# Kernel tuning notes

Measured on AMD Instinct MI355X. Metric: run time of the kernel, lower is better.

The kernel has to match this reference:

```python
import jax, jax.numpy as jnp
import numpy as np

B, N_FEAT, D = 16384, 32, 64
HID1, HID2, HOF = 1024, 512, 64
OUT = 1
N_PAIRS = N_FEAT * (N_FEAT - 1) // 2
EPS = 1e-5


def setup_inputs() -> dict:
    key = jax.random.key(0)
    ks = jax.random.split(key, 16)
    s = 0.02
    return {
        "x": jax.random.normal(ks[0], (B, N_FEAT, D), dtype=jnp.float32),
        "W1": jax.random.normal(ks[1], (N_FEAT * D, HID1), dtype=jnp.float32) * s,
        "b1": jnp.zeros((HID1,), jnp.float32),
        "g1": jnp.ones((HID1,), jnp.float32),
        "beta1": jnp.zeros((HID1,), jnp.float32),
        "W2": jax.random.normal(ks[2], (HID1, HID2), dtype=jnp.float32) * s,
        "b2": jnp.zeros((HID2,), jnp.float32),
        "g2": jnp.ones((HID2,), jnp.float32),
        "beta2": jnp.zeros((HID2,), jnp.float32),
        "W3": jax.random.normal(ks[3], (HID2, HOF), dtype=jnp.float32) * s,
        "b3": jnp.zeros((HOF,), jnp.float32),
        "Wc": jax.random.normal(ks[4], (HOF + N_PAIRS, OUT), dtype=jnp.float32) * s,
        "bc": jnp.zeros((OUT,), jnp.float32),
    }


def _batchnorm(h, g, beta):
    # BatchNorm1d in training mode: batch mean / biased variance
    m = jnp.mean(h, axis=0)
    v = jnp.var(h, axis=0)
    return g * (h - m) * jax.lax.rsqrt(v + EPS) + beta


_IU, _JU = np.triu_indices(N_FEAT, k=1)  # same (i<j) order as nested loop


def reference(x, W1, b1, g1, beta1, W2, b2, g2, beta2, W3, b3, Wc, bc):
    # second-order interactions: all pairwise dot products, gathered upper-tri
    gram = jnp.einsum("bnd,bmd->bnm", x, x)          # [B, N, N]
    pairs = gram[:, _IU, _JU]                          # [B, N*(N-1)/2]
    # deep processor
    flat = x.reshape(x.shape[0], -1)                   # [B, N*D]
    h = _batchnorm(jax.nn.relu(flat @ W1 + b1), g1, beta1)
    h = _batchnorm(jax.nn.relu(h @ W2 + b2), g2, beta2)
    hof = h @ W3 + b3                                  # [B, HOF]
    inter = jnp.concatenate([hof, pairs], axis=1)
    return inter @ Wc + bc
```

## Files before the change

kernel.cpp:

```cpp
#include <hip/hip_runtime.h>
#include <stdint.h>

typedef unsigned short u16;
typedef unsigned char u8;
typedef __attribute__((ext_vector_type(8))) short short8;
typedef __attribute__((ext_vector_type(4))) float f32x4;
typedef __attribute__((ext_vector_type(16))) float f32x16;
typedef __attribute__((ext_vector_type(4))) int i32x4;
typedef __attribute__((ext_vector_type(8))) int i32x8;

#define BATCH 16384L
#define WSCALE 64.0f
#define INV_WSCALE (1.0f / 64.0f)
#define SCALE_ONE 0x7f7f7f7f
#define INVB (1.0f / 16384.0f)

__device__ __forceinline__ u16 f2bf_trunc(float f) {
    union { float f; uint32_t u; } cv; cv.f = f;
    return (u16)(cv.u >> 16);
}
__device__ __forceinline__ float bf2f(u16 h) {
    union { uint32_t u; float f; } cv; cv.u = ((uint32_t)h) << 16;
    return cv.f;
}
template<bool HI>
__device__ __forceinline__ uint32_t fp8pk(float a, float b, uint32_t old) {
    return (uint32_t)__builtin_amdgcn_cvt_pk_fp8_f32(a, b, (int)old, HI);
}
__device__ __forceinline__ u8 f2fp8(float v) {
    return (u8)(__builtin_amdgcn_cvt_pk_fp8_f32(v, v, 0, false) & 0xff);
}

__global__ __launch_bounds__(256) void k_gram(const float* __restrict__ x,
                                              const float* __restrict__ Wc,
                                              const float* __restrict__ W1,
                                              u8* __restrict__ xb,
                                              u8* __restrict__ w1f,
                                              float* __restrict__ spair,
                                              float* __restrict__ stats) {
    if (blockIdx.x >= 4096) {
        __shared__ float tile[32][33];
        const int bid2 = blockIdx.x - 4096;
        const int nb = (bid2 & 31) * 32;
        const int kb = (bid2 >> 5) * 32;
        const int tx = threadIdx.x & 31, ty = threadIdx.x >> 5;
        for (int r = ty; r < 32; r += 8)
            tile[r][tx] = W1[(long)(kb + r) * 1024 + nb + tx];
        __syncthreads();
        for (int r = ty; r < 32; r += 8)
            w1f[(long)(nb + r) * 2048 + kb + tx] = f2fp8(WSCALE * tile[tx][r]);
        return;
    }
    if (blockIdx.x == 0) {
        for (int j = threadIdx.x; j < 3072; j += 256) stats[j] = 0.f;
    }
    const int wave = threadIdx.x >> 6;
    const int lane = threadIdx.x & 63;
    const long b = (long)blockIdx.x * 4 + wave;
    const int r16 = lane & 15, quad = lane >> 4;
    const float* xg = x + b * 2048;

    short8 hi[2][2], lo[2][2];
    for (int mt = 0; mt < 2; mt++) {
        for (int k0 = 0; k0 < 2; k0++) {
            const int row = mt * 16 + r16;
            const int kof = k0 * 32 + quad * 8;
            const float* p = xg + row * 64 + kof;
            float4 p0 = *(const float4*)p;
            float4 p1 = *(const float4*)(p + 4);
            float v[8] = {p0.x, p0.y, p0.z, p0.w, p1.x, p1.y, p1.z, p1.w};
            short8 h, l;
            for (int j = 0; j < 8; j++) {
                u16 hb = f2bf_trunc(v[j]);
                h[j] = (short)hb;
                l[j] = (short)f2bf_trunc(v[j] - bf2f(hb));
            }
            hi[mt][k0] = h; lo[mt][k0] = l;
            uint32_t w0 = fp8pk<false>(v[0], v[1], 0); w0 = fp8pk<true>(v[2], v[3], w0);
            uint32_t w1 = fp8pk<false>(v[4], v[5], 0); w1 = fp8pk<true>(v[6], v[7], w1);
            *(uint2*)(xb + b * 2048 + row * 64 + kof) = make_uint2(w0, w1);
        }
    }
    f32x4 zero = {0.f, 0.f, 0.f, 0.f};
    f32x4 acc[2][2];
    for (int mt = 0; mt < 2; mt++) for (int nt = 0; nt < 2; nt++) acc[mt][nt] = zero;
    for (int k0 = 0; k0 < 2; k0++)
        for (int mt = 0; mt < 2; mt++)
            for (int nt = 0; nt < 2; nt++) {
                acc[mt][nt] = __builtin_amdgcn_mfma_f32_16x16x32_bf16(hi[mt][k0], hi[nt][k0], acc[mt][nt], 0, 0, 0);
                acc[mt][nt] = __builtin_amdgcn_mfma_f32_16x16x32_bf16(hi[mt][k0], lo[nt][k0], acc[mt][nt], 0, 0, 0);
                acc[mt][nt] = __builtin_amdgcn_mfma_f32_16x16x32_bf16(lo[mt][k0], hi[nt][k0], acc[mt][nt], 0, 0, 0);
            }
    float pacc = 0.f;
    for (int mt = 0; mt < 2; mt++)
        for (int nt = 0; nt < 2; nt++)
            for (int r = 0; r < 4; r++) {
                int row = mt * 16 + quad * 4 + r;
                int col = nt * 16 + r16;
                if (col > row) {
                    int p = 31 * row - (row * (row - 1)) / 2 + (col - row - 1);
                    pacc += acc[mt][nt][r] * Wc[64 + p];
                }
            }
    for (int off = 1; off < 64; off <<= 1) pacc += __shfl_xor(pacc, off);
    if (lane == 0) spair[b] = pacc;
}

__device__ __forceinline__ i32x8 frag32(const u8* __restrict__ lds, int R, int cb) {
    const int s = R & 7;
    i32x4 lo = *(const i32x4*)&lds[R * 128 + ((cb ^ s) * 16)];
    i32x4 hi = *(const i32x4*)&lds[R * 128 + (((cb + 1) ^ s) * 16)];
    i32x8 r;
    r[0] = lo[0]; r[1] = lo[1]; r[2] = lo[2]; r[3] = lo[3];
    r[4] = hi[0]; r[5] = hi[1]; r[6] = hi[2]; r[7] = hi[3];
    return r;
}

template<int LOGNB>
__global__ __launch_bounds__(512) void gemm_bn8(const u8* __restrict__ A,
                                                const u8* __restrict__ Bt,
                                                const float* __restrict__ bias,
                                                u8* __restrict__ C,
                                                float* __restrict__ sums,
                                                float* __restrict__ ssq,
                                                int N, int K, float inv) {
    __shared__ u8 lA[2][32768];
    __shared__ u8 lB[2][32768];
    const int tid = threadIdx.x;
    const int lane = tid & 63, wave = tid >> 6;
    const int wm = wave >> 2, wn = wave & 3;
    const int r32 = lane & 31, hf = lane >> 5;
    const int lid = blockIdx.x;
    const int xcd = lid & 7, t = lid >> 3;
    const int nbk = t & ((1 << LOGNB) - 1);
    const int mbk = xcd * (32 >> LOGNB) + (t >> LOGNB);
    const long m0 = (long)mbk * 256;
    const long n0 = (long)nbk * 256;

    const u8* srcA[4]; const u8* srcB[4]; int dstc[4];
#pragma unroll
    for (int i = 0; i < 4; i++) {
        const int c = tid + 512 * i;
        const int row = c >> 3, pos = c & 7;
        const int g = pos ^ (row & 7);
        srcA[i] = A + (m0 + row) * (long)K + g * 16;
        srcB[i] = Bt + (n0 + row) * (long)K + g * 16;
        dstc[i] = c * 16;
    }

    f32x16 acc[4][2];
#pragma unroll
    for (int mt = 0; mt < 4; mt++)
#pragma unroll
        for (int nt = 0; nt < 2; nt++)
#pragma unroll
            for (int r = 0; r < 16; r++) acc[mt][nt][r] = 0.f;

#pragma unroll
    for (int i = 0; i < 4; i++)
        __builtin_amdgcn_global_load_lds((const __attribute__((address_space(1))) void*)srcA[i],
                                         (__attribute__((address_space(3))) void*)(&lA[0][dstc[i]]), 16, 0, 0);
#pragma unroll
    for (int i = 0; i < 4; i++)
        __builtin_amdgcn_global_load_lds((const __attribute__((address_space(1))) void*)srcB[i],
                                         (__attribute__((address_space(3))) void*)(&lB[0][dstc[i]]), 16, 0, 0);
    __syncthreads();

    const int NT = K >> 7;
    for (int ti = 0; ti < NT; ti++) {
        const int cur = ti & 1, nxt = cur ^ 1;
        const long koff = (long)(ti + 1) << 7;
        const bool pf = (ti + 1 < NT);
        const u8* la = &lA[cur][0];
        const u8* lb = &lB[cur][0];
        i32x8 af[4], bf;

#pragma unroll
        for (int mt = 0; mt < 4; mt++)
            af[mt] = frag32(la, wm * 128 + mt * 32 + r32, hf * 2);
        bf = frag32(lb, wn * 64 + r32, hf * 2);
        if (pf) {
#pragma unroll
            for (int i = 0; i < 4; i++)
                __builtin_amdgcn_global_load_lds((const __attribute__((address_space(1))) void*)(srcA[i] + koff),
                                                 (__attribute__((address_space(3))) void*)(&lA[nxt][dstc[i]]), 16, 0, 0);
        }
        __builtin_amdgcn_s_barrier();
        asm volatile("s_waitcnt lgkmcnt(0)" ::: "memory");
        __builtin_amdgcn_sched_barrier(0);
        __builtin_amdgcn_s_setprio(1);
#pragma unroll
        for (int mt = 0; mt < 4; mt++)
            acc[mt][0] = __builtin_amdgcn_mfma_scale_f32_32x32x64_f8f6f4(
                af[mt], bf, acc[mt][0], 0, 0, 0, SCALE_ONE, 0, SCALE_ONE);
        __builtin_amdgcn_s_setprio(0);
        __builtin_amdgcn_s_barrier();

        bf = frag32(lb, wn * 64 + 32 + r32, hf * 2);
        if (pf) {
#pragma unroll
            for (int i = 0; i < 4; i++)
                __builtin_amdgcn_global_load_lds((const __attribute__((address_space(1))) void*)(srcB[i] + koff),
                                                 (__attribute__((address_space(3))) void*)(&lB[nxt][dstc[i]]), 16, 0, 0);
        }
        __builtin_amdgcn_s_barrier();
        asm volatile("s_waitcnt lgkmcnt(0)" ::: "memory");
        __builtin_amdgcn_sched_barrier(0);
        __builtin_amdgcn_s_setprio(1);
#pragma unroll
        for (int mt = 0; mt < 4; mt++)
            acc[mt][1] = __builtin_amdgcn_mfma_scale_f32_32x32x64_f8f6f4(
                af[mt], bf, acc[mt][1], 0, 0, 0, SCALE_ONE, 0, SCALE_ONE);
        __builtin_amdgcn_s_setprio(0);
        __builtin_amdgcn_s_barrier();

#pragma unroll
        for (int mt = 0; mt < 4; mt++)
            af[mt] = frag32(la, wm * 128 + mt * 32 + r32, 4 + hf * 2);
        bf = frag32(lb, wn * 64 + r32, 4 + hf * 2);
        __builtin_amdgcn_s_barrier();
        asm volatile("s_waitcnt lgkmcnt(0)" ::: "memory");
        __builtin_amdgcn_sched_barrier(0);
        __builtin_amdgcn_s_setprio(1);
#pragma unroll
        for (int mt = 0; mt < 4; mt++)
            acc[mt][0] = __builtin_amdgcn_mfma_scale_f32_32x32x64_f8f6f4(
                af[mt], bf, acc[mt][0], 0, 0, 0, SCALE_ONE, 0, SCALE_ONE);
        __builtin_amdgcn_s_setprio(0);
        __builtin_amdgcn_s_barrier();

        bf = frag32(lb, wn * 64 + 32 + r32, 4 + hf * 2);
        __builtin_amdgcn_s_barrier();
        asm volatile("s_waitcnt lgkmcnt(0)" ::: "memory");
        __builtin_amdgcn_sched_barrier(0);
        __builtin_amdgcn_s_setprio(1);
#pragma unroll
        for (int mt = 0; mt < 4; mt++)
            acc[mt][1] = __builtin_amdgcn_mfma_scale_f32_32x32x64_f8f6f4(
                af[mt], bf, acc[mt][1], 0, 0, 0, SCALE_ONE, 0, SCALE_ONE);
        __builtin_amdgcn_s_setprio(0);
        asm volatile("s_waitcnt vmcnt(0)" ::: "memory");
        __builtin_amdgcn_s_barrier();
    }

#pragma unroll
    for (int nt = 0; nt < 2; nt++) {
        const int col = (int)n0 + wn * 64 + nt * 32 + r32;
        const float bcol = bias[col];
        float s = 0.f, sq = 0.f;
#pragma unroll
        for (int mt = 0; mt < 4; mt++)
#pragma unroll
            for (int r = 0; r < 16; r++) {
                const long row = m0 + wm * 128 + mt * 32 + 4 * hf + (r & 3) + 8 * (r >> 2);
                float v = acc[mt][nt][r] * inv + bcol;
                v = fmaxf(v, 0.f);
                C[row * N + col] = f2fp8(v);
                s += v; sq += v * v;
            }
        s += __shfl_xor(s, 32);
        sq += __shfl_xor(sq, 32);
        if (hf == 0) { atomicAdd(&sums[col], s); atomicAdd(&ssq[col], sq); }
    }
}

template<int LOGNB>
__global__ __launch_bounds__(256) void gemm_bn(const u8* __restrict__ A,
                                               const u8* __restrict__ Bt,
                                               const float* __restrict__ bias,
                                               u8* __restrict__ C,
                                               float* __restrict__ sums,
                                               float* __restrict__ ssq,
                                               int N, int K, float inv) {
    __shared__ u8 lA[128 * 128];
    __shared__ u8 lB[128 * 128];
    const int tid = threadIdx.x;
    const int lane = tid & 63, wave = tid >> 6;
    const int wm = wave >> 1, wn = wave & 1;
    const int r32 = lane & 31, hf = lane >> 5;
    const int lid = blockIdx.x;
    const int xcd = lid & 7, t = lid >> 3;
    const int nbk = t & ((1 << LOGNB) - 1);
    const int mbk = (xcd << 4) + (t >> LOGNB);
    const long m0 = (long)mbk * 128;
    const long n0 = (long)nbk * 128;

    f32x16 acc[2][2];
    for (int mt = 0; mt < 2; mt++)
        for (int nt = 0; nt < 2; nt++)
            for (int r = 0; r < 16; r++) acc[mt][nt][r] = 0.f;

    for (long k0 = 0; k0 < K; k0 += 128) {
        __syncthreads();
        for (int i = 0; i < 4; i++) {
            const int c = tid + 256 * i;
            const int row = c >> 3, pos = c & 7;
            const int g = pos ^ (row & 7);
            const u8* ga = A + (m0 + row) * K + k0 + g * 16;
            const u8* gb = Bt + (n0 + row) * K + k0 + g * 16;
            __builtin_amdgcn_global_load_lds((const __attribute__((address_space(1))) void*)ga,
                                             (__attribute__((address_space(3))) void*)(&lA[c * 16]), 16, 0, 0);
            __builtin_amdgcn_global_load_lds((const __attribute__((address_space(1))) void*)gb,
                                             (__attribute__((address_space(3))) void*)(&lB[c * 16]), 16, 0, 0);
        }
        __syncthreads();
        for (int km = 0; km < 2; km++) {
            const int cb = km * 4 + hf * 2;
            i32x8 af[2], bfr[2];
            for (int mt = 0; mt < 2; mt++)
                af[mt] = frag32(lA, wm * 64 + mt * 32 + r32, cb);
            for (int nt = 0; nt < 2; nt++)
                bfr[nt] = frag32(lB, wn * 64 + nt * 32 + r32, cb);
            for (int mt = 0; mt < 2; mt++)
                for (int nt = 0; nt < 2; nt++)
                    acc[mt][nt] = __builtin_amdgcn_mfma_scale_f32_32x32x64_f8f6f4(
                        af[mt], bfr[nt], acc[mt][nt], 0, 0,
                        0, SCALE_ONE, 0, SCALE_ONE);
        }
    }

    for (int nt = 0; nt < 2; nt++) {
        const int col = (int)n0 + wn * 64 + nt * 32 + r32;
        const float bcol = bias[col];
        float s = 0.f, sq = 0.f;
        for (int mt = 0; mt < 2; mt++)
            for (int r = 0; r < 16; r++) {
                const long row = m0 + wm * 64 + mt * 32 + 4 * hf + (r & 3) + 8 * (r >> 2);
                float v = acc[mt][nt][r] * inv + bcol;
                v = fmaxf(v, 0.f);
                C[row * N + col] = f2fp8(v);
                s += v; sq += v * v;
            }
        s += __shfl_xor(s, 32);
        sq += __shfl_xor(sq, 32);
        if (hf == 0) { atomicAdd(&sums[col], s); atomicAdd(&ssq[col], sq); }
    }
}

__global__ __launch_bounds__(256) void k_mid(const float* __restrict__ sums1,
                                             const float* __restrict__ ssq1,
                                             const float* __restrict__ g1,
                                             const float* __restrict__ beta1,
                                             const float* __restrict__ W2,
                                             const float* __restrict__ b2,
                                             u8* __restrict__ w2f,
                                             float* __restrict__ b2a,
                                             const float* __restrict__ W3,
                                             const float* __restrict__ b3,
                                             const float* __restrict__ Wc,
                                             const float* __restrict__ bc,
                                             float* __restrict__ vv,
                                             float* __restrict__ c0) {
    const int bid = blockIdx.x;
    if (bid < 512) {
        __shared__ float tile[32][33];
        __shared__ float sc[32];
        const int nb = (bid & 15) * 32;
        const int kb = (bid >> 4) * 32;
        const int tx = threadIdx.x & 31, ty = threadIdx.x >> 5;
        if (threadIdx.x < 32) {
            const int k = kb + threadIdx.x;
            const float m = sums1[k] * INVB;
            const float var = ssq1[k] * INVB - m * m;
            sc[threadIdx.x] = g1[k] * rsqrtf(var + 1e-5f);
        }
        __syncthreads();
        for (int r = ty; r < 32; r += 8)
            tile[r][tx] = sc[r] * W2[(long)(kb + r) * 512 + nb + tx];
        __syncthreads();
        for (int r = ty; r < 32; r += 8)
            w2f[(long)(nb + r) * 1024 + kb + tx] = f2fp8(WSCALE * tile[tx][r]);
    } else if (bid < 520) {
        __shared__ float c1s[1024];
        __shared__ float part[4][64];
        for (int k = threadIdx.x; k < 1024; k += 256) {
            const float m = sums1[k] * INVB;
            const float var = ssq1[k] * INVB - m * m;
            const float a = g1[k] * rsqrtf(var + 1e-5f);
            c1s[k] = beta1[k] - a * m;
        }
        __syncthreads();
        const int lane = threadIdx.x & 63, w = threadIdx.x >> 6;
        const int col = (bid - 512) * 64 + lane;
        float s = 0.f;
        for (int k = w * 256; k < w * 256 + 256; k++)
            s += c1s[k] * W2[(long)k * 512 + col];
        part[w][lane] = s;
        __syncthreads();
        if (w == 0)
            b2a[col] = b2[col] + part[0][lane] + part[1][lane] + part[2][lane] + part[3][lane];
    } else {
        for (int k = threadIdx.x; k < 512; k += 256) {
            float s = 0.f;
            for (int j = 0; j < 64; j++) s += W3[k * 64 + j] * Wc[j];
            vv[k] = s;
        }
        if (threadIdx.x == 0) {
            float s = 0.f;
            for (int j = 0; j < 64; j++) s += b3[j] * Wc[j];
            *c0 = s + bc[0];
        }
    }
}

__global__ __launch_bounds__(256) void k_final(const u8* __restrict__ h2,
                                               const float* __restrict__ sums2,
                                               const float* __restrict__ ssq2,
                                               const float* __restrict__ g2,
                                               const float* __restrict__ beta2,
                                               const float* __restrict__ v,
                                               const float* __restrict__ c0,
                                               const float* __restrict__ spair,
                                               float* __restrict__ out) {
    const int wave = threadIdx.x >> 6, lane = threadIdx.x & 63;
    const long b = (long)blockIdx.x * 4 + wave;
    const int k0 = lane * 8;
    uint2 hv = *(const uint2*)&h2[b * 512 + k0];
    float f[8];
    f[0] = __builtin_amdgcn_cvt_f32_fp8(hv.x, 0);
    f[1] = __builtin_amdgcn_cvt_f32_fp8(hv.x, 1);
    f[2] = __builtin_amdgcn_cvt_f32_fp8(hv.x, 2);
    f[3] = __builtin_amdgcn_cvt_f32_fp8(hv.x, 3);
    f[4] = __builtin_amdgcn_cvt_f32_fp8(hv.y, 0);
    f[5] = __builtin_amdgcn_cvt_f32_fp8(hv.y, 1);
    f[6] = __builtin_amdgcn_cvt_f32_fp8(hv.y, 2);
    f[7] = __builtin_amdgcn_cvt_f32_fp8(hv.y, 3);
    float4 sm0 = *(const float4*)&sums2[k0], sm1 = *(const float4*)&sums2[k0 + 4];
    float4 sq0 = *(const float4*)&ssq2[k0],  sq1 = *(const float4*)&ssq2[k0 + 4];
    float4 gg0 = *(const float4*)&g2[k0],    gg1 = *(const float4*)&g2[k0 + 4];
    float4 bb0 = *(const float4*)&beta2[k0], bb1 = *(const float4*)&beta2[k0 + 4];
    float4 vv0 = *(const float4*)&v[k0],     vv1 = *(const float4*)&v[k0 + 4];
    float sm[8] = {sm0.x, sm0.y, sm0.z, sm0.w, sm1.x, sm1.y, sm1.z, sm1.w};
    float sq[8] = {sq0.x, sq0.y, sq0.z, sq0.w, sq1.x, sq1.y, sq1.z, sq1.w};
    float gg[8] = {gg0.x, gg0.y, gg0.z, gg0.w, gg1.x, gg1.y, gg1.z, gg1.w};
    float bb[8] = {bb0.x, bb0.y, bb0.z, bb0.w, bb1.x, bb1.y, bb1.z, bb1.w};
    float vk[8] = {vv0.x, vv0.y, vv0.z, vv0.w, vv1.x, vv1.y, vv1.z, vv1.w};
    float acc = 0.f;
#pragma unroll
    for (int j = 0; j < 8; j++) {
        const float m = sm[j] * INVB;
        const float var = sq[j] * INVB - m * m;
        const float a = gg[j] * rsqrtf(var + 1e-5f);
        const float c = bb[j] - a * m;
        acc += (a * f[j] + c) * vk[j];
    }
    for (int off = 1; off < 64; off <<= 1) acc += __shfl_xor(acc, off);
    if (lane == 0) out[b] = acc + spair[b] + c0[0];
}

extern "C" void kernel_launch(void* const* d_in, const int* in_sizes, int n_in,
                              void* d_out, int out_size, void* d_ws, size_t ws_size,
                              hipStream_t stream) {
    const float* x     = (const float*)d_in[0];
    const float* W1    = (const float*)d_in[1];
    const float* b1    = (const float*)d_in[2];
    const float* g1    = (const float*)d_in[3];
    const float* beta1 = (const float*)d_in[4];
    const float* W2    = (const float*)d_in[5];
    const float* b2    = (const float*)d_in[6];
    const float* g2    = (const float*)d_in[7];
    const float* beta2 = (const float*)d_in[8];
    const float* W3    = (const float*)d_in[9];
    const float* b3    = (const float*)d_in[10];
    const float* Wc    = (const float*)d_in[11];
    const float* bc    = (const float*)d_in[12];
    float* out = (float*)d_out;

    char* ws = (char*)d_ws;
    size_t o = 0;
    u8* xb  = (u8*)(ws + o); o += BATCH * 2048;
    u8* w1f = (u8*)(ws + o); o += 2048L * 1024;
    u8* w2f = (u8*)(ws + o); o += 1024L * 512;
    u8* h1b = (u8*)(ws + o); o += BATCH * 1024;
    u8* h2b = (u8*)(ws + o); o += BATCH * 512;
    float* spair = (float*)(ws + o); o += BATCH * 4;
    float* stats = (float*)(ws + o); o += 3072 * 4;
    float* sums1 = stats, *ssq1 = stats + 1024, *sums2 = stats + 2048, *ssq2 = stats + 2560;
    float* vv = (float*)(ws + o); o += 512 * 4;
    float* c0 = (float*)(ws + o); o += 4;
    float* b2a = (float*)(ws + o); o += 512 * 4;

    k_gram<<<6144, 256, 0, stream>>>(x, Wc, W1, xb, w1f, spair, stats);
    gemm_bn8<2><<<256, 512, 0, stream>>>(xb, w1f, b1, h1b, sums1, ssq1, 1024, 2048, INV_WSCALE);
    k_mid<<<521, 256, 0, stream>>>(sums1, ssq1, g1, beta1, W2, b2, w2f, b2a,
                                   W3, b3, Wc, bc, vv, c0);
    gemm_bn<2><<<512, 256, 0, stream>>>(h1b, w2f, b2a, h2b, sums2, ssq2, 512, 1024, INV_WSCALE);
    k_final<<<4096, 256, 0, stream>>>(h2b, sums2, ssq2, g2, beta2, vv, c0, spair, out);
}
```

Before: 299.5 us.

## Replace both FP8 GEMMs with a unified triple-buffered K=64 pipelined kernel

Both FP8 GEMMs now use one templated kernel that keeps a three-stage ring of 64-wide K slices in LDS, prefetching two tiles ahead and waiting with counted vmcnt so loads overlap MFMA work. The K step shrinks from 128 to 64 and the LDS swizzle is changed to match. The second GEMM moves from 128x128 tiles with 256 threads and no prefetch to 256x128 tiles with 512 threads and the same pipeline. This adds one barrier per 64-wide K step and depends on the hand-written vmcnt counts being correct.

```diff
diff --git a/kernel.cpp b/kernel.cpp
--- a/kernel.cpp
+++ b/kernel.cpp
@@ -106,146 +106,134 @@
     if (lane == 0) spair[b] = pacc;
 }
 
-__device__ __forceinline__ i32x8 frag32(const u8* __restrict__ lds, int R, int cb) {
-    const int s = R & 7;
-    i32x4 lo = *(const i32x4*)&lds[R * 128 + ((cb ^ s) * 16)];
-    i32x4 hi = *(const i32x4*)&lds[R * 128 + (((cb + 1) ^ s) * 16)];
+__device__ __forceinline__ i32x8 frag64(const u8* __restrict__ lds, int R, int cb) {
+    const int s = (R & 3) ^ ((R >> 2) & 3);
+    i32x4 lo = *(const i32x4*)&lds[R * 64 + ((cb ^ s) * 16)];
+    i32x4 hi = *(const i32x4*)&lds[R * 64 + (((cb + 1) ^ s) * 16)];
     i32x8 r;
     r[0] = lo[0]; r[1] = lo[1]; r[2] = lo[2]; r[3] = lo[3];
     r[4] = hi[0]; r[5] = hi[1]; r[6] = hi[2]; r[7] = hi[3];
     return r;
 }
 
-template<int LOGNB>
-__global__ __launch_bounds__(512) void gemm_bn8(const u8* __restrict__ A,
-                                                const u8* __restrict__ Bt,
-                                                const float* __restrict__ bias,
-                                                u8* __restrict__ C,
-                                                float* __restrict__ sums,
-                                                float* __restrict__ ssq,
-                                                int N, int K, float inv) {
-    __shared__ u8 lA[2][32768];
-    __shared__ u8 lB[2][32768];
+template<int NTB>
+__global__ __launch_bounds__(512) void gemm_pipe(const u8* __restrict__ A,
+                                                 const u8* __restrict__ Bt,
+                                                 const float* __restrict__ bias,
+                                                 u8* __restrict__ C,
+                                                 float* __restrict__ sums,
+                                                 float* __restrict__ ssq,
+                                                 int N, int K, float inv) {
+    __shared__ u8 lA[3 * 16384];
+    __shared__ u8 lB[3 * 8192 * NTB];
     const int tid = threadIdx.x;
     const int lane = tid & 63, wave = tid >> 6;
     const int wm = wave >> 2, wn = wave & 3;
     const int r32 = lane & 31, hf = lane >> 5;
     const int lid = blockIdx.x;
-    const int xcd = lid & 7, t = lid >> 3;
-    const int nbk = t & ((1 << LOGNB) - 1);
-    const int mbk = xcd * (32 >> LOGNB) + (t >> LOGNB);
+    const int xcd = lid & 7, t8 = lid >> 3;
+    const int nbk = t8 & 3;
+    const int mbk = xcd * 8 + (t8 >> 2);
     const long m0 = (long)mbk * 256;
-    const long n0 = (long)nbk * 256;
-
-    const u8* srcA[4]; const u8* srcB[4]; int dstc[4];
-#pragma unroll
-    for (int i = 0; i < 4; i++) {
+    const long n0 = (long)nbk * (128 * NTB);
+
+    const u8* srcA[2]; int dca[2];
+#pragma unroll
+    for (int i = 0; i < 2; i++) {
         const int c = tid + 512 * i;
-        const int row = c >> 3, pos = c & 7;
-        const int g = pos ^ (row & 7);
+        const int row = c >> 2, pos = c & 3;
+        const int g = pos ^ ((row & 3) ^ ((row >> 2) & 3));
         srcA[i] = A + (m0 + row) * (long)K + g * 16;
+        dca[i] = c * 16;
+    }
+    const u8* srcB[NTB]; int dcb[NTB];
+#pragma unroll
+    for (int i = 0; i < NTB; i++) {
+        const int c = tid + 512 * i;
+        const int row = c >> 2, pos = c & 3;
+        const int g = pos ^ ((row & 3) ^ ((row >> 2) & 3));
         srcB[i] = Bt + (n0 + row) * (long)K + g * 16;
-        dstc[i] = c * 16;
-    }
-
-    f32x16 acc[4][2];
+        dcb[i] = c * 16;
+    }
+
+    f32x16 acc[4][NTB];
 #pragma unroll
     for (int mt = 0; mt < 4; mt++)
 #pragma unroll
-        for (int nt = 0; nt < 2; nt++)
+        for (int nt = 0; nt < NTB; nt++)
 #pragma unroll
             for (int r = 0; r < 16; r++) acc[mt][nt][r] = 0.f;
 
 #pragma unroll
-    for (int i = 0; i < 4; i++)
-        __builtin_amdgcn_global_load_lds((const __attribute__((address_space(1))) void*)srcA[i],
-                                         (__attribute__((address_space(3))) void*)(&lA[0][dstc[i]]), 16, 0, 0);
-#pragma unroll
-    for (int i = 0; i < 4; i++)
-        __builtin_amdgcn_global_load_lds((const __attribute__((address_space(1))) void*)srcB[i],
-                                         (__attribute__((address_space(3))) void*)(&lB[0][dstc[i]]), 16, 0, 0);
-    __syncthreads();
-
-    const int NT = K >> 7;
-    for (int ti = 0; ti < NT; ti++) {
-        const int cur = ti & 1, nxt = cur ^ 1;
-        const long koff = (long)(ti + 1) << 7;
-        const bool pf = (ti + 1 < NT);
-        const u8* la = &lA[cur][0];
-        const u8* lb = &lB[cur][0];
-        i32x8 af[4], bf;
-
+    for (int st = 0; st < 2; st++) {
+        const long ko = (long)st << 6;
+        u8* da = &lA[st * 16384];
+        u8* db = &lB[st * (8192 * NTB)];
+#pragma unroll
+        for (int i = 0; i < 2; i++)
+            __builtin_amdgcn_global_load_lds((const __attribute__((address_space(1))) void*)(srcA[i] + ko),
+                                             (__attribute__((address_space(3))) void*)(da + dca[i]), 16, 0, 0);
+#pragma unroll
+        for (int i = 0; i < NTB; i++)
+            __builtin_amdgcn_global_load_lds((const __attribute__((address_space(1))) void*)(srcB[i] + ko),
+                                             (__attribute__((address_space(3))) void*)(db + dcb[i]), 16, 0, 0);
+    }
+
+    const int NT = K >> 6;
+    int rb = 0, wb = 2;
+    for (int t = 0; t < NT; ++t) {
+        if (t + 2 < NT) {
+            const long ko = (long)(t + 2) << 6;
+            u8* da = &lA[wb * 16384];
+            u8* db = &lB[wb * (8192 * NTB)];
+#pragma unroll
+            for (int i = 0; i < 2; i++)
+                __builtin_amdgcn_global_load_lds((const __attribute__((address_space(1))) void*)(srcA[i] + ko),
+                                                 (__attribute__((address_space(3))) void*)(da + dca[i]), 16, 0, 0);
+#pragma unroll
+            for (int i = 0; i < NTB; i++)
+                __builtin_amdgcn_global_load_lds((const __attribute__((address_space(1))) void*)(srcB[i] + ko),
+                                                 (__attribute__((address_space(3))) void*)(db + dcb[i]), 16, 0, 0);
+            if constexpr (NTB == 2) asm volatile("s_waitcnt vmcnt(8)" ::: "memory");
+            else                    asm volatile("s_waitcnt vmcnt(6)" ::: "memory");
+        } else if (t + 2 == NT) {
+            if constexpr (NTB == 2) asm volatile("s_waitcnt vmcnt(4)" ::: "memory");
+            else                    asm volatile("s_waitcnt vmcnt(3)" ::: "memory");
+        } else {
+            asm volatile("s_waitcnt vmcnt(0)" ::: "memory");
+        }
+        __builtin_amdgcn_s_barrier();
+        asm volatile("" ::: "memory");
+
+        const u8* la = &lA[rb * 16384];
+        const u8* lb = &lB[rb * (8192 * NTB)];
+        const int cb = hf * 2;
+        i32x8 af[4], bf[NTB];
 #pragma unroll
         for (int mt = 0; mt < 4; mt++)
-            af[mt] = frag32(la, wm * 128 + mt * 32 + r32, hf * 2);
-        bf = frag32(lb, wn * 64 + r32, hf * 2);
-        if (pf) {
-#pragma unroll
-            for (int i = 0; i < 4; i++)
-                __builtin_amdgcn_global_load_lds((const __attribute__((address_space(1))) void*)(srcA[i] + koff),
-                                                 (__attribute__((address_space(3))) void*)(&lA[nxt][dstc[i]]), 16, 0, 0);
-        }
-        __builtin_amdgcn_s_barrier();
+            af[mt] = frag64(la, wm * 128 + mt * 32 + r32, cb);
+#pragma unroll
+        for (int nt = 0; nt < NTB; nt++)
+            bf[nt] = frag64(lb, wn * (32 * NTB) + nt * 32 + r32, cb);
         asm volatile("s_waitcnt lgkmcnt(0)" ::: "memory");
         __builtin_amdgcn_sched_barrier(0);
         __builtin_amdgcn_s_setprio(1);
 #pragma unroll
         for (int mt = 0; mt < 4; mt++)
-            acc[mt][0] = __builtin_amdgcn_mfma_scale_f32_32x32x64_f8f6f4(
-                af[mt], bf, acc[mt][0], 0, 0, 0, SCALE_ONE, 0, SCALE_ONE);
+#pragma unroll
+            for (int nt = 0; nt < NTB; nt++)
+                acc[mt][nt] = __builtin_amdgcn_mfma_scale_f32_32x32x64_f8f6f4(
+                    af[mt], bf[nt], acc[mt][nt], 0, 0, 0, SCALE_ONE, 0, SCALE_ONE);
         __builtin_amdgcn_s_setprio(0);
         __builtin_amdgcn_s_barrier();
-
-        bf = frag32(lb, wn * 64 + 32 + r32, hf * 2);
-        if (pf) {
-#pragma unroll
-            for (int i = 0; i < 4; i++)
-                __builtin_amdgcn_global_load_lds((const __attribute__((address_space(1))) void*)(srcB[i] + koff),
-                                                 (__attribute__((address_space(3))) void*)(&lB[nxt][dstc[i]]), 16, 0, 0);
-        }
-        __builtin_amdgcn_s_barrier();
-        asm volatile("s_waitcnt lgkmcnt(0)" ::: "memory");
-        __builtin_amdgcn_sched_barrier(0);
-        __builtin_amdgcn_s_setprio(1);
-#pragma unroll
-        for (int mt = 0; mt < 4; mt++)
-            acc[mt][1] = __builtin_amdgcn_mfma_scale_f32_32x32x64_f8f6f4(
-                af[mt], bf, acc[mt][1], 0, 0, 0, SCALE_ONE, 0, SCALE_ONE);
-        __builtin_amdgcn_s_setprio(0);
-        __builtin_amdgcn_s_barrier();
-
-#pragma unroll
-        for (int mt = 0; mt < 4; mt++)
-            af[mt] = frag32(la, wm * 128 + mt * 32 + r32, 4 + hf * 2);
-        bf = frag32(lb, wn * 64 + r32, 4 + hf * 2);
-        __builtin_amdgcn_s_barrier();
-        asm volatile("s_waitcnt lgkmcnt(0)" ::: "memory");
-        __builtin_amdgcn_sched_barrier(0);
-        __builtin_amdgcn_s_setprio(1);
-#pragma unroll
-        for (int mt = 0; mt < 4; mt++)
-            acc[mt][0] = __builtin_amdgcn_mfma_scale_f32_32x32x64_f8f6f4(
-                af[mt], bf, acc[mt][0], 0, 0, 0, SCALE_ONE, 0, SCALE_ONE);
-        __builtin_amdgcn_s_setprio(0);
-        __builtin_amdgcn_s_barrier();
-
-        bf = frag32(lb, wn * 64 + 32 + r32, 4 + hf * 2);
-        __builtin_amdgcn_s_barrier();
-        asm volatile("s_waitcnt lgkmcnt(0)" ::: "memory");
-        __builtin_amdgcn_sched_barrier(0);
-        __builtin_amdgcn_s_setprio(1);
-#pragma unroll
-        for (int mt = 0; mt < 4; mt++)
-            acc[mt][1] = __builtin_amdgcn_mfma_scale_f32_32x32x64_f8f6f4(
-                af[mt], bf, acc[mt][1], 0, 0, 0, SCALE_ONE, 0, SCALE_ONE);
-        __builtin_amdgcn_s_setprio(0);
-        asm volatile("s_waitcnt vmcnt(0)" ::: "memory");
-        __builtin_amdgcn_s_barrier();
-    }
-
-#pragma unroll
-    for (int nt = 0; nt < 2; nt++) {
-        const int col = (int)n0 + wn * 64 + nt * 32 + r32;
+        asm volatile("" ::: "memory");
+        rb = rb == 2 ? 0 : rb + 1;
+        wb = wb == 2 ? 0 : wb + 1;
+    }
+
+#pragma unroll
+    for (int nt = 0; nt < NTB; nt++) {
+        const int col = (int)n0 + wn * (32 * NTB) + nt * 32 + r32;
         const float bcol = bias[col];
         float s = 0.f, sq = 0.f;
 #pragma unroll
@@ -253,79 +241,6 @@
 #pragma unroll
             for (int r = 0; r < 16; r++) {
                 const long row = m0 + wm * 128 + mt * 32 + 4 * hf + (r & 3) + 8 * (r >> 2);
-                float v = acc[mt][nt][r] * inv + bcol;
-                v = fmaxf(v, 0.f);
-                C[row * N + col] = f2fp8(v);
-                s += v; sq += v * v;
-            }
-        s += __shfl_xor(s, 32);
-        sq += __shfl_xor(sq, 32);
-        if (hf == 0) { atomicAdd(&sums[col], s); atomicAdd(&ssq[col], sq); }
-    }
-}
-
-template<int LOGNB>
-__global__ __launch_bounds__(256) void gemm_bn(const u8* __restrict__ A,
-                                               const u8* __restrict__ Bt,
-                                               const float* __restrict__ bias,
-                                               u8* __restrict__ C,
-                                               float* __restrict__ sums,
-                                               float* __restrict__ ssq,
-                                               int N, int K, float inv) {
-    __shared__ u8 lA[128 * 128];
-    __shared__ u8 lB[128 * 128];
-    const int tid = threadIdx.x;
-    const int lane = tid & 63, wave = tid >> 6;
-    const int wm = wave >> 1, wn = wave & 1;
-    const int r32 = lane & 31, hf = lane >> 5;
-    const int lid = blockIdx.x;
-    const int xcd = lid & 7, t = lid >> 3;
-    const int nbk = t & ((1 << LOGNB) - 1);
-    const int mbk = (xcd << 4) + (t >> LOGNB);
-    const long m0 = (long)mbk * 128;
-    const long n0 = (long)nbk * 128;
-
-    f32x16 acc[2][2];
-    for (int mt = 0; mt < 2; mt++)
-        for (int nt = 0; nt < 2; nt++)
-            for (int r = 0; r < 16; r++) acc[mt][nt][r] = 0.f;
-
-    for (long k0 = 0; k0 < K; k0 += 128) {
-        __syncthreads();
-        for (int i = 0; i < 4; i++) {
-            const int c = tid + 256 * i;
-            const int row = c >> 3, pos = c & 7;
-            const int g = pos ^ (row & 7);
-            const u8* ga = A + (m0 + row) * K + k0 + g * 16;
-            const u8* gb = Bt + (n0 + row) * K + k0 + g * 16;
-            __builtin_amdgcn_global_load_lds((const __attribute__((address_space(1))) void*)ga,
-                                             (__attribute__((address_space(3))) void*)(&lA[c * 16]), 16, 0, 0);
-            __builtin_amdgcn_global_load_lds((const __attribute__((address_space(1))) void*)gb,
-                                             (__attribute__((address_space(3))) void*)(&lB[c * 16]), 16, 0, 0);
-        }
-        __syncthreads();
-        for (int km = 0; km < 2; km++) {
-            const int cb = km * 4 + hf * 2;
-            i32x8 af[2], bfr[2];
-            for (int mt = 0; mt < 2; mt++)
-                af[mt] = frag32(lA, wm * 64 + mt * 32 + r32, cb);
-            for (int nt = 0; nt < 2; nt++)
-                bfr[nt] = frag32(lB, wn * 64 + nt * 32 + r32, cb);
-            for (int mt = 0; mt < 2; mt++)
-                for (int nt = 0; nt < 2; nt++)
-                    acc[mt][nt] = __builtin_amdgcn_mfma_scale_f32_32x32x64_f8f6f4(
-                        af[mt], bfr[nt], acc[mt][nt], 0, 0,
-                        0, SCALE_ONE, 0, SCALE_ONE);
-        }
-    }
-
-    for (int nt = 0; nt < 2; nt++) {
-        const int col = (int)n0 + wn * 64 + nt * 32 + r32;
-        const float bcol = bias[col];
-        float s = 0.f, sq = 0.f;
-        for (int mt = 0; mt < 2; mt++)
-            for (int r = 0; r < 16; r++) {
-                const long row = m0 + wm * 64 + mt * 32 + 4 * hf + (r & 3) + 8 * (r >> 2);
                 float v = acc[mt][nt][r] * inv + bcol;
                 v = fmaxf(v, 0.f);
                 C[row * N + col] = f2fp8(v);
@@ -481,9 +396,9 @@
     float* b2a = (float*)(ws + o); o += 512 * 4;
 
     k_gram<<<6144, 256, 0, stream>>>(x, Wc, W1, xb, w1f, spair, stats);
-    gemm_bn8<2><<<256, 512, 0, stream>>>(xb, w1f, b1, h1b, sums1, ssq1, 1024, 2048, INV_WSCALE);
+    gemm_pipe<2><<<256, 512, 0, stream>>>(xb, w1f, b1, h1b, sums1, ssq1, 1024, 2048, INV_WSCALE);
     k_mid<<<521, 256, 0, stream>>>(sums1, ssq1, g1, beta1, W2, b2, w2f, b2a,
                                    W3, b3, Wc, bc, vv, c0);
-    gemm_bn<2><<<512, 256, 0, stream>>>(h1b, w2f, b2a, h2b, sums2, ssq2, 512, 1024, INV_WSCALE);
+    gemm_pipe<1><<<256, 512, 0, stream>>>(h1b, w2f, b2a, h2b, sums2, ssq2, 512, 1024, INV_WSCALE);
     k_final<<<4096, 256, 0, stream>>>(h2b, sums2, ssq2, g2, beta2, vv, c0, spair, out);
 }
```

New measurement: 306.1 us. 1.02x slower.
